# Performance work log

Hardware: AMD Instinct MI355X
Metric: run time of the kernel (lower is better)

The kernel has to match this reference:

```python
import jax, jax.numpy as jnp
import numpy as np

N = 50000      # nodes
E = 800000     # edges (avg degree 16)
C_IN = 256
C_OUT = 256
H = 4
D = C_OUT // H  # 64
NEG_SLOPE = 0.2


def setup_inputs() -> dict:
    key = jax.random.key(0)
    ks = jax.random.split(key, 12)
    glorot = lambda k, shape: jax.random.uniform(k, shape, jnp.float32, -1.0, 1.0) * np.sqrt(6.0 / (shape[0] + shape[1]))
    return {
        "x": jax.random.normal(ks[0], (N, C_IN), jnp.float32),
        "src": jax.random.randint(ks[1], (E,), 0, N, jnp.int32),
        "dst": jax.random.randint(ks[2], (E,), 0, N, jnp.int32),
        "Wl": glorot(ks[3], (C_IN, C_OUT)),
        "bl": jnp.zeros((C_OUT,), jnp.float32),
        "Wr": glorot(ks[4], (C_IN, C_OUT)),
        "br": jnp.zeros((C_OUT,), jnp.float32),
        "Wv": glorot(ks[5], (C_IN, C_OUT)),
        "bv": jnp.zeros((C_OUT,), jnp.float32),
        "att_l": jax.random.normal(ks[6], (1, H, D), jnp.float32) * 0.1,
        "att_r": jax.random.normal(ks[7], (1, H, D), jnp.float32) * 0.1,
    }


def reference(x, src, dst, Wl, bl, Wr, br, Wv, bv, att_l, att_r):
    # lambda_policy=None, gcn_mode=False -> lmbda = lmbda2 = 1.0
    n = x.shape[0]
    sl = ((x @ Wl + bl).reshape(n, H, D) * att_l).sum(-1, keepdims=True)  # [N,H,1]
    sr = ((x @ Wr + br).reshape(n, H, D) * att_r).sum(-1, keepdims=True)  # [N,H,1]
    xv = (x @ Wv + bv).reshape(n, H, D)                                    # [N,H,D]

    # --- convolve branch: average scores over in-neighborhood (incl. self) ---
    hlr = jnp.concatenate([sl, sr], axis=1)                   # [N,2H,1]
    conv = jax.ops.segment_sum(hlr[src], dst, num_segments=n)  # sum_{u->v} hsrc[u]
    deg = jax.ops.segment_sum(jnp.ones((src.shape[0],), x.dtype), dst, num_segments=n)
    agg = (hlr + conv) / (1.0 + deg[:, None, None])            # [N,2H,1]
    sl, sr = agg[:, :H], agg[:, H:]

    # --- edge attention: gather-add-leakyrelu, segment softmax over dst ---
    e = jax.nn.leaky_relu(sl[src] + sr[dst], NEG_SLOPE)        # [E,H,1]
    emax = jax.ops.segment_max(e, dst, num_segments=n)
    emax = jnp.where(jnp.isfinite(emax), emax, 0.0)
    ex = jnp.exp(e - emax[dst])
    denom = jax.ops.segment_sum(ex, dst, num_segments=n)
    a = ex / jnp.maximum(denom[dst], 1e-16)                    # [E,H,1]

    # --- weighted message aggregation ---
    out = jax.ops.segment_sum(xv[src] * a, dst, num_segments=n)  # [N,H,D]
    return out
```

## Files before the change

kernel.cpp:

```cpp
#include <hip/hip_runtime.h>

#define C_IN 256
#define C_OUT 256
#define NH 4
#define HD 64
#define NEG_SLOPE 0.2f

typedef _Float16 half8 __attribute__((ext_vector_type(8)));
typedef _Float16 half4v __attribute__((ext_vector_type(4)));
typedef float floatx4 __attribute__((ext_vector_type(4)));

__global__ void make_eff_w(const float* __restrict__ Wl, const float* __restrict__ Wr,
                           const float* __restrict__ bl, const float* __restrict__ br,
                           const float* __restrict__ attl, const float* __restrict__ attr,
                           float* __restrict__ Ws, float* __restrict__ bs)
{
    int c = blockIdx.x;
    int t = threadIdx.x;
    int h = t >> 6, d = t & 63;
    float al = attl[t], ar = attr[t];
    float vl, vr;
    if (c < C_IN) { vl = Wl[c * C_OUT + t] * al; vr = Wr[c * C_OUT + t] * ar; }
    else          { vl = bl[t] * al;             vr = br[t] * ar; }
#pragma unroll
    for (int off = 32; off >= 1; off >>= 1) {
        vl += __shfl_xor(vl, off, 64);
        vr += __shfl_xor(vr, off, 64);
    }
    if (d == 0) {
        if (c < C_IN) { Ws[c * 8 + h] = vl; Ws[c * 8 + 4 + h] = vr; }
        else          { bs[h] = vl;         bs[4 + h] = vr; }
    }
}

__global__ void transpose_w(const float* __restrict__ Wv, _Float16* __restrict__ WvT)
{
    int idx = blockIdx.x * 256 + threadIdx.x;
    int n = idx >> 8, k = idx & 255;
    WvT[n * 256 + k] = (_Float16)Wv[k * 256 + n];
}

__global__ __launch_bounds__(256) void node_scores(const float* __restrict__ x,
    const float* __restrict__ Ws, const float* __restrict__ bs,
    float* __restrict__ s, int N)
{
    int lane = threadIdx.x & 63, wid = threadIdx.x >> 6;
    float w[4][8];
#pragma unroll
    for (int i = 0; i < 4; ++i)
#pragma unroll
        for (int jq = 0; jq < 2; ++jq) {
            float4 v = *(const float4*)(Ws + (4 * lane + i) * 8 + jq * 4);
            w[i][jq * 4 + 0] = v.x; w[i][jq * 4 + 1] = v.y;
            w[i][jq * 4 + 2] = v.z; w[i][jq * 4 + 3] = v.w;
        }
    float b0[8];
#pragma unroll
    for (int j = 0; j < 8; ++j) b0[j] = bs[j];

    int wglob = blockIdx.x * 4 + wid;
    int nwaves = gridDim.x * 4;
    for (int n = wglob; n < N; n += nwaves) {
        float4 xv4 = *(const float4*)(x + (size_t)n * 256 + 4 * lane);
        float acc[8];
#pragma unroll
        for (int j = 0; j < 8; ++j)
            acc[j] = xv4.x * w[0][j] + xv4.y * w[1][j] + xv4.z * w[2][j] + xv4.w * w[3][j];
#pragma unroll
        for (int off = 32; off >= 1; off >>= 1)
#pragma unroll
            for (int j = 0; j < 8; ++j) acc[j] += __shfl_xor(acc[j], off, 64);
        if (lane == 0) {
            *(float4*)(s + (size_t)n * 8)     = make_float4(acc[0] + b0[0], acc[1] + b0[1], acc[2] + b0[2], acc[3] + b0[3]);
            *(float4*)(s + (size_t)n * 8 + 4) = make_float4(acc[4] + b0[4], acc[5] + b0[5], acc[6] + b0[6], acc[7] + b0[7]);
        }
    }
}

__global__ __launch_bounds__(256) void gemm_xv(const float* __restrict__ x,
    const _Float16* __restrict__ WvT, const float* __restrict__ bv,
    _Float16* __restrict__ xv, int M)
{
    __shared__ __align__(16) _Float16 As[128][40];
    __shared__ __align__(16) _Float16 Bs[128][40];
    int tid = threadIdx.x;
    int wid = tid >> 6, lane = tid & 63;
    int quad = lane >> 4, r16 = lane & 15;
    int m0 = blockIdx.x * 128, n0 = blockIdx.y * 128;

    floatx4 acc[2][8];
#pragma unroll
    for (int i = 0; i < 2; ++i)
#pragma unroll
        for (int j = 0; j < 8; ++j) acc[i][j] = (floatx4){0.f, 0.f, 0.f, 0.f};

    int arow = tid >> 3, af4 = tid & 7;
    int brow = tid >> 2, bg  = tid & 3;

    for (int k0 = 0; k0 < 256; k0 += 32) {
#pragma unroll
        for (int p = 0; p < 4; ++p) {
            int rr = arow + p * 32;
            int gm = m0 + rr;
            float4 v = make_float4(0.f, 0.f, 0.f, 0.f);
            if (gm < M) v = *(const float4*)(x + (size_t)gm * 256 + k0 + af4 * 4);
            _Float16* dp = &As[rr][af4 * 4];
            dp[0] = (_Float16)v.x; dp[1] = (_Float16)v.y;
            dp[2] = (_Float16)v.z; dp[3] = (_Float16)v.w;
        }
#pragma unroll
        for (int p = 0; p < 2; ++p) {
            int nr = brow + p * 64;
            *(float4*)&Bs[nr][bg * 8] = *(const float4*)(WvT + (size_t)(n0 + nr) * 256 + k0 + bg * 8);
        }
        __syncthreads();
        half8 a[2], b[8];
#pragma unroll
        for (int rg = 0; rg < 2; ++rg)
            a[rg] = *(const half8*)&As[wid * 32 + rg * 16 + r16][quad * 8];
#pragma unroll
        for (int cg = 0; cg < 8; ++cg)
            b[cg] = *(const half8*)&Bs[cg * 16 + r16][quad * 8];
#pragma unroll
        for (int rg = 0; rg < 2; ++rg)
#pragma unroll
            for (int cg = 0; cg < 8; ++cg)
                acc[rg][cg] = __builtin_amdgcn_mfma_f32_16x16x32_f16(a[rg], b[cg], acc[rg][cg], 0, 0, 0);
        __syncthreads();
    }
#pragma unroll
    for (int rg = 0; rg < 2; ++rg) {
        int rbase = m0 + wid * 32 + rg * 16 + quad * 4;
#pragma unroll
        for (int cg = 0; cg < 8; ++cg) {
            int gcol = n0 + cg * 16 + r16;
            float bias = bv[gcol];
#pragma unroll
            for (int rr = 0; rr < 4; ++rr) {
                int grow = rbase + rr;
                if (grow < M)
                    xv[(size_t)grow * 256 + gcol] = (_Float16)(acc[rg][cg][rr] + bias);
            }
        }
    }
}

__global__ void deg_kernel(const int* __restrict__ dst, int* __restrict__ deg, int E)
{
    int i = blockIdx.x * 256 + threadIdx.x;
    if (i < E) atomicAdd(&deg[dst[i]], 1);
}

__global__ void scan_part(const int* __restrict__ deg, int* __restrict__ partials,
                          int N, int chunk)
{
    __shared__ int sd[256];
    int b = blockIdx.x, t = threadIdx.x;
    int idx = b * chunk + t;
    int v = (t < chunk && idx < N) ? deg[idx] : 0;
    sd[t] = v; __syncthreads();
    for (int off = 128; off >= 1; off >>= 1) {
        if (t < off) sd[t] += sd[t + off];
        __syncthreads();
    }
    if (t == 0) partials[b] = sd[0];
}

__global__ void scan_partials(const int* __restrict__ partials, int* __restrict__ pscan)
{
    __shared__ int sd[256];
    int t = threadIdx.x;
    int v = partials[t];
    sd[t] = v; __syncthreads();
    for (int off = 1; off < 256; off <<= 1) {
        int x = (t >= off) ? sd[t - off] : 0;
        __syncthreads();
        sd[t] += x;
        __syncthreads();
    }
    pscan[t] = sd[t] - v;
}

__global__ void scan_final(const int* __restrict__ deg, const int* __restrict__ pscan,
                           int* __restrict__ offs, int N, int chunk)
{
    __shared__ int sd[256];
    int b = blockIdx.x, t = threadIdx.x;
    int idx = b * chunk + t;
    int v = (t < chunk && idx < N) ? deg[idx] : 0;
    sd[t] = v; __syncthreads();
    for (int off = 1; off < 256; off <<= 1) {
        int x = (t >= off) ? sd[t - off] : 0;
        __syncthreads();
        sd[t] += x;
        __syncthreads();
    }
    int incl = sd[t], excl = incl - v;
    int base = pscan[b];
    if (t < chunk && idx < N) offs[idx] = base + excl;
    if (idx == N - 1) offs[N] = base + incl;
}

__global__ void scatter_kernel(const int* __restrict__ src, const int* __restrict__ dst,
                               const int* __restrict__ offs, int* __restrict__ cursor,
                               int* __restrict__ csr_src, int E)
{
    int i = blockIdx.x * 256 + threadIdx.x;
    if (i < E) {
        int d = dst[i];
        int p = offs[d] + atomicAdd(&cursor[d], 1);
        csr_src[p] = src[i];
    }
}

__global__ void agg_kernel(const float* __restrict__ s, const int* __restrict__ csr_src,
                           const int* __restrict__ offs, const int* __restrict__ deg,
                           float* __restrict__ aggl, float* __restrict__ aggr, int N)
{
    int gid = blockIdx.x * 256 + threadIdx.x;
    int n = gid >> 3, c = gid & 7;
    if (n >= N) return;
    int off = offs[n], dg = deg[n];
    float acc = s[(size_t)n * 8 + c];
    int i = 0;
    for (; i + 4 <= dg; i += 4) {
        int p0 = csr_src[off + i];
        int p1 = csr_src[off + i + 1];
        int p2 = csr_src[off + i + 2];
        int p3 = csr_src[off + i + 3];
        float v0 = s[(size_t)p0 * 8 + c];
        float v1 = s[(size_t)p1 * 8 + c];
        float v2 = s[(size_t)p2 * 8 + c];
        float v3 = s[(size_t)p3 * 8 + c];
        acc += (v0 + v1) + (v2 + v3);
    }
    for (; i < dg; ++i) acc += s[(size_t)csr_src[off + i] * 8 + c];
    acc *= 1.0f / (1.0f + (float)dg);
    if (c < 4) aggl[(size_t)n * 4 + c]     = acc;
    else       aggr[(size_t)n * 4 + c - 4] = acc;
}

template<int SZ>
__device__ __forceinline__ void attn_chunk(
    const int* __restrict__ csr_base, const float* __restrict__ aggl,
    float ar, int myedge, int grp, int myhead, int lane,
    const _Float16* __restrict__ xv,
    float& denom, float& o0, float& o1, float& o2, float& o3)
{
    int cs = 0;
    float wexp = 0.f;
    if (myedge < SZ) {
        cs = csr_base[myedge];
        float e = aggl[(size_t)cs * 4 + myhead] + ar;
        e = (e > 0.f) ? e : NEG_SLOPE * e;
        wexp = __expf(e);
    }
    denom += wexp;
#pragma unroll
    for (int j = 0; j < SZ; ++j) {
        int   sidx = __shfl(cs, j, 64);
        float w    = __shfl(wexp, grp + j, 64);
        half4v hv  = *(const half4v*)(xv + (size_t)sidx * 256 + lane * 4);
        o0 += w * (float)hv[0];
        o1 += w * (float)hv[1];
        o2 += w * (float)hv[2];
        o3 += w * (float)hv[3];
    }
}

__global__ __launch_bounds__(256) void attn_out(const float* __restrict__ aggl,
    const float* __restrict__ aggr, const int* __restrict__ csr_src,
    const int* __restrict__ offs, const int* __restrict__ deg,
    const _Float16* __restrict__ xv, float* __restrict__ out, int N)
{
    int wid = threadIdx.x >> 6, lane = threadIdx.x & 63;
    int n = blockIdx.x * 4 + wid;
    if (n >= N) return;
    int myhead = lane >> 4, myedge = lane & 15, grp = lane & 48;
    int off = offs[n], dg = deg[n];
    float ar = aggr[(size_t)n * 4 + myhead];

    float denom = 0.f, o0 = 0.f, o1 = 0.f, o2 = 0.f, o3 = 0.f;
    int i0 = 0;
    for (; i0 + 16 <= dg; i0 += 16)
        attn_chunk<16>(csr_src + off + i0, aggl, ar, myedge, grp, myhead, lane, xv, denom, o0, o1, o2, o3);
    int rem = dg - i0;
    if (rem & 8) {
        attn_chunk<8>(csr_src + off + i0, aggl, ar, myedge, grp, myhead, lane, xv, denom, o0, o1, o2, o3);
        i0 += 8;
    }
    if (rem & 4) {
        attn_chunk<4>(csr_src + off + i0, aggl, ar, myedge, grp, myhead, lane, xv, denom, o0, o1, o2, o3);
        i0 += 4;
    }
    if (rem & 2) {
        attn_chunk<2>(csr_src + off + i0, aggl, ar, myedge, grp, myhead, lane, xv, denom, o0, o1, o2, o3);
        i0 += 2;
    }
    if (rem & 1) {
        attn_chunk<1>(csr_src + off + i0, aggl, ar, myedge, grp, myhead, lane, xv, denom, o0, o1, o2, o3);
    }

#pragma unroll
    for (int o = 1; o <= 8; o <<= 1) denom += __shfl_xor(denom, o, 64);
    float inv = 1.0f / fmaxf(denom, 1e-16f);
    *(float4*)(out + (size_t)n * 256 + lane * 4) = make_float4(o0 * inv, o1 * inv, o2 * inv, o3 * inv);
}

extern "C" void kernel_launch(void* const* d_in, const int* in_sizes, int n_in,
                              void* d_out, int out_size, void* d_ws, size_t ws_size,
                              hipStream_t stream)
{
    const float* x    = (const float*)d_in[0];
    const int*   src  = (const int*)d_in[1];
    const int*   dst  = (const int*)d_in[2];
    const float* Wl   = (const float*)d_in[3];
    const float* bl   = (const float*)d_in[4];
    const float* Wr   = (const float*)d_in[5];
    const float* br   = (const float*)d_in[6];
    const float* Wv   = (const float*)d_in[7];
    const float* bv   = (const float*)d_in[8];
    const float* attl = (const float*)d_in[9];
    const float* attr = (const float*)d_in[10];
    float* out = (float*)d_out;

    int N = in_sizes[0] / C_IN;
    int E = in_sizes[1];

    char* p = (char*)d_ws;
    auto alloc = [&](size_t bytes) -> void* {
        uintptr_t q = (uintptr_t)p;
        q = (q + 255) & ~(uintptr_t)255;
        p = (char*)(q + bytes);
        return (void*)q;
    };
    float* Ws     = (float*)alloc((size_t)C_IN * 8 * sizeof(float));
    float* bs     = (float*)alloc(8 * sizeof(float));
    float* s      = (float*)alloc((size_t)N * 8 * sizeof(float));
    float* aggl   = (float*)alloc((size_t)N * 4 * sizeof(float));
    float* aggr   = (float*)alloc((size_t)N * 4 * sizeof(float));
    int* deg      = (int*)alloc((size_t)N * sizeof(int));
    int* offs     = (int*)alloc((size_t)(N + 1) * sizeof(int));
    int* cursor   = (int*)alloc((size_t)N * sizeof(int));
    int* partials = (int*)alloc(256 * sizeof(int));
    int* pscan    = (int*)alloc(256 * sizeof(int));
    int* csr_src  = (int*)alloc((size_t)E * sizeof(int));
    _Float16* WvT = (_Float16*)alloc((size_t)C_IN * C_OUT * sizeof(_Float16));
    _Float16* xv  = (_Float16*)alloc((size_t)N * C_OUT * sizeof(_Float16));

    hipMemsetAsync(deg, 0, (size_t)N * sizeof(int), stream);
    hipMemsetAsync(cursor, 0, (size_t)N * sizeof(int), stream);

    make_eff_w<<<C_IN + 1, 256, 0, stream>>>(Wl, Wr, bl, br, attl, attr, Ws, bs);
    transpose_w<<<(C_IN * C_OUT) / 256, 256, 0, stream>>>(Wv, WvT);
    node_scores<<<768, 256, 0, stream>>>(x, Ws, bs, s, N);
    gemm_xv<<<dim3((N + 127) / 128, C_OUT / 128), 256, 0, stream>>>(x, WvT, bv, xv, N);
    deg_kernel<<<(E + 255) / 256, 256, 0, stream>>>(dst, deg, E);
    int chunk = (N + 255) / 256;
    scan_part<<<256, 256, 0, stream>>>(deg, partials, N, chunk);
    scan_partials<<<1, 256, 0, stream>>>(partials, pscan);
    scan_final<<<256, 256, 0, stream>>>(deg, pscan, offs, N, chunk);
    scatter_kernel<<<(E + 255) / 256, 256, 0, stream>>>(src, dst, offs, cursor, csr_src, E);
    agg_kernel<<<(N * 8 + 255) / 256, 256, 0, stream>>>(s, csr_src, offs, deg, aggl, aggr, N);
    attn_out<<<(N + 3) / 4, 256, 0, stream>>>(aggl, aggr, csr_src, offs, deg, xv, out, N);
}
```

Measured before the change: 351.5 us.

## Software-pipeline edge-score loads in attention kernel with persistent grid-stride waves

Replaces the chunked 16/8/4/2/1 remainder dispatch in the attention-aggregation kernel with one 16-edge loop that prefetches the next chunk's source indices and exp-scores while the current chunk's features are accumulated. The kernel becomes a persistent grid-stride loop over 2048 blocks instead of one wave per node. It also uses 32-bit index arithmetic and a nontemporal output store. The intent is to hide the gather latency of csr_src/aggl behind the xv accumulation and cut launch overhead. The cost is that every partial chunk now runs a full 16-iteration loop with zero weights, wasting xv loads of row 0, and the fixed grid may limit occupancy.

```diff
diff --git a/kernel.cpp b/kernel.cpp
--- a/kernel.cpp
+++ b/kernel.cpp
@@ -240,71 +240,59 @@
     else       aggr[(size_t)n * 4 + c - 4] = acc;
 }
 
-template<int SZ>
-__device__ __forceinline__ void attn_chunk(
-    const int* __restrict__ csr_base, const float* __restrict__ aggl,
-    float ar, int myedge, int grp, int myhead, int lane,
-    const _Float16* __restrict__ xv,
-    float& denom, float& o0, float& o1, float& o2, float& o3)
-{
-    int cs = 0;
-    float wexp = 0.f;
-    if (myedge < SZ) {
-        cs = csr_base[myedge];
-        float e = aggl[(size_t)cs * 4 + myhead] + ar;
-        e = (e > 0.f) ? e : NEG_SLOPE * e;
-        wexp = __expf(e);
-    }
-    denom += wexp;
-#pragma unroll
-    for (int j = 0; j < SZ; ++j) {
-        int   sidx = __shfl(cs, j, 64);
-        float w    = __shfl(wexp, grp + j, 64);
-        half4v hv  = *(const half4v*)(xv + (size_t)sidx * 256 + lane * 4);
-        o0 += w * (float)hv[0];
-        o1 += w * (float)hv[1];
-        o2 += w * (float)hv[2];
-        o3 += w * (float)hv[3];
-    }
-}
-
 __global__ __launch_bounds__(256) void attn_out(const float* __restrict__ aggl,
     const float* __restrict__ aggr, const int* __restrict__ csr_src,
     const int* __restrict__ offs, const int* __restrict__ deg,
     const _Float16* __restrict__ xv, float* __restrict__ out, int N)
 {
     int wid = threadIdx.x >> 6, lane = threadIdx.x & 63;
-    int n = blockIdx.x * 4 + wid;
-    if (n >= N) return;
     int myhead = lane >> 4, myedge = lane & 15, grp = lane & 48;
-    int off = offs[n], dg = deg[n];
-    float ar = aggr[(size_t)n * 4 + myhead];
-
-    float denom = 0.f, o0 = 0.f, o1 = 0.f, o2 = 0.f, o3 = 0.f;
-    int i0 = 0;
-    for (; i0 + 16 <= dg; i0 += 16)
-        attn_chunk<16>(csr_src + off + i0, aggl, ar, myedge, grp, myhead, lane, xv, denom, o0, o1, o2, o3);
-    int rem = dg - i0;
-    if (rem & 8) {
-        attn_chunk<8>(csr_src + off + i0, aggl, ar, myedge, grp, myhead, lane, xv, denom, o0, o1, o2, o3);
-        i0 += 8;
-    }
-    if (rem & 4) {
-        attn_chunk<4>(csr_src + off + i0, aggl, ar, myedge, grp, myhead, lane, xv, denom, o0, o1, o2, o3);
-        i0 += 4;
-    }
-    if (rem & 2) {
-        attn_chunk<2>(csr_src + off + i0, aggl, ar, myedge, grp, myhead, lane, xv, denom, o0, o1, o2, o3);
-        i0 += 2;
-    }
-    if (rem & 1) {
-        attn_chunk<1>(csr_src + off + i0, aggl, ar, myedge, grp, myhead, lane, xv, denom, o0, o1, o2, o3);
-    }
-
-#pragma unroll
-    for (int o = 1; o <= 8; o <<= 1) denom += __shfl_xor(denom, o, 64);
-    float inv = 1.0f / fmaxf(denom, 1e-16f);
-    *(float4*)(out + (size_t)n * 256 + lane * 4) = make_float4(o0 * inv, o1 * inv, o2 * inv, o3 * inv);
+    int nwaves = gridDim.x * 4;
+
+    for (int n = blockIdx.x * 4 + wid; n < N; n += nwaves) {
+        int off = offs[n], dg = deg[n];
+        float ar = aggr[(unsigned)(n * 4 + myhead)];
+
+        float denom = 0.f, o0 = 0.f, o1 = 0.f, o2 = 0.f, o3 = 0.f;
+
+        int cs = 0; float wexp = 0.f;
+        if (myedge < dg) {
+            cs = csr_src[off + myedge];
+            float e = aggl[(unsigned)((cs << 2) + myhead)] + ar;
+            e = (e > 0.f) ? e : NEG_SLOPE * e;
+            wexp = __expf(e);
+        }
+
+        for (int b = 0; b < dg; b += 16) {
+            int   cs_c = cs;
+            float w_c  = wexp;
+            cs = 0; wexp = 0.f;
+            int nb = b + 16;
+            if (nb + myedge < dg) {
+                cs = csr_src[off + nb + myedge];
+                float e = aggl[(unsigned)((cs << 2) + myhead)] + ar;
+                e = (e > 0.f) ? e : NEG_SLOPE * e;
+                wexp = __expf(e);
+            }
+            denom += w_c;
+#pragma unroll
+            for (int j = 0; j < 16; ++j) {
+                int   sidx = __shfl(cs_c, j, 64);
+                float w    = __shfl(w_c, grp + j, 64);
+                const half4v hv = *(const half4v*)(xv + (unsigned)((sidx << 8) | (lane << 2)));
+                o0 += w * (float)hv[0];
+                o1 += w * (float)hv[1];
+                o2 += w * (float)hv[2];
+                o3 += w * (float)hv[3];
+            }
+        }
+
+#pragma unroll
+        for (int o = 1; o <= 8; o <<= 1) denom += __shfl_xor(denom, o, 64);
+        float inv = 1.0f / fmaxf(denom, 1e-16f);
+        floatx4 res = {o0 * inv, o1 * inv, o2 * inv, o3 * inv};
+        __builtin_nontemporal_store(res, (floatx4*)(out + (size_t)n * 256 + (lane << 2)));
+    }
 }
 
 extern "C" void kernel_launch(void* const* d_in, const int* in_sizes, int n_in,
@@ -362,5 +350,5 @@
     scan_final<<<256, 256, 0, stream>>>(deg, pscan, offs, N, chunk);
     scatter_kernel<<<(E + 255) / 256, 256, 0, stream>>>(src, dst, offs, cursor, csr_src, E);
     agg_kernel<<<(N * 8 + 255) / 256, 256, 0, stream>>>(s, csr_src, offs, deg, aggl, aggr, N);
-    attn_out<<<(N + 3) / 4, 256, 0, stream>>>(aggl, aggr, csr_src, offs, deg, xv, out, N);
-}
+    attn_out<<<2048, 256, 0, stream>>>(aggl, aggr, csr_src, offs, deg, xv, out, N);
+}
```

Result: no change. 351.0 us (-0.1%).
